# Kernel tuning notes

Hardware: AMD Instinct MI355X
Metric: run time of the kernel (lower is better)

Reference implementation:

```python
import jax, jax.numpy as jnp
import numpy as np

KH = KW = 3  # fixed: distortion() generates a 9-tap (3x3) offset grid


def make_offset(h, w, dilation=1.0, skydome=True):
    """Faithful numpy port of DistortionConvLayer.distortion -> [1,h,w,9,2] (last dim = [x_off, y_off])."""
    pi = np.pi
    unit_w = 2.0 * pi / w
    unit_h = pi / (2.0 * h) if skydome else pi / h
    rho = np.tan(unit_w) * dilation
    v = np.array([0.0, 1.0, 0.0])
    r_grid = np.array([[1, -1], [1, 0], [1, 1], [0, -1], [0, 0], [0, 1], [-1, -1], [-1, 0], [-1, 1]], dtype=np.float64)
    xc = int(w * 0.5)
    theta = (xc - 0.5 * w) * unit_w
    y = np.arange(h, dtype=np.float64)
    phi = (h - y) * unit_h if skydome else (h * 0.5 - y) * unit_h  # [h]
    p_u = np.stack([np.cos(phi) * np.cos(theta), np.sin(phi), np.cos(phi) * np.sin(theta)], axis=-1)  # [h,3]
    t_x = np.cross(np.broadcast_to(v, p_u.shape), p_u)  # [h,3]
    t_y = np.cross(p_u, t_x)                            # [h,3]
    # r_sphere: [h,9,3]
    r_sphere = rho * (r_grid[None, :, 0, None] * t_x[:, None, :] + r_grid[None, :, 1, None] * t_y[:, None, :])
    p_ur = p_u[:, None, :] + r_sphere  # [h,9,3]
    ux, uy, uz = p_ur[..., 0], p_ur[..., 1], p_ur[..., 2]
    base = np.arctan2(uz, ux)
    theta_r = np.where(ux > 0, base,
               np.where(ux < 0, np.where(uz >= 0, base + pi, base - pi),
                np.where(uz > 0, pi * 0.5, -pi * 0.5)))
    phi_r = np.arcsin(uy)
    x_r = (theta_r / pi + 1.0) * 0.5 * w
    y_r = (1.0 - 2.0 * phi_r / pi) * h if skydome else (0.5 - phi_r / pi) * h
    k = np.stack([x_r, y_r], axis=-1)          # [h,9,2], entries [x, y] (as in original)
    off = k - k[:, 4:5, :]                      # subtract center tap
    off = np.broadcast_to(off[:, None, :, :], (h, w, 9, 2))  # tile over width
    return off[None].astype(np.float32)         # [1,h,w,9,2]


def setup_inputs() -> dict:
    key = jax.random.key(0)
    k1, k2 = jax.random.split(key)
    B, H, W, C, F = 4, 128, 256, 64, 128
    inputs = jax.random.normal(k1, (B, H, W, C), dtype=jnp.float32)
    fan_in = KH * KW * C
    kernel = jax.random.normal(k2, (fan_in, F), dtype=jnp.float32) * (1.0 / np.sqrt(fan_in))
    bias = jnp.zeros((F,), dtype=jnp.float32)
    return {"inputs": inputs, "kernel": kernel, "bias": bias}


def reference(inputs, kernel, bias):
    B, H, W, C = inputs.shape
    F = kernel.shape[1]
    off = jnp.asarray(make_offset(H, W))  # [1,H,W,9,2], static constant
    # 'same' padding for 3x3, stride 1, dilation 1 -> pad 1 on each side
    xp = jnp.pad(inputs, ((0, 0), (1, 1), (1, 1), (0, 0)))
    in_h, in_w = H + 2, W + 2
    # base conv sampling coordinates (extract_patches order: tap k -> dy=k//3, dx=k%3)
    dy = jnp.repeat(jnp.arange(KH), KW).astype(jnp.float32)  # [9]
    dx = jnp.tile(jnp.arange(KW), KH).astype(jnp.float32)    # [9]
    base_y = jnp.arange(H, dtype=jnp.float32)[None, :, None, None] + dy[None, None, None, :]  # [1,H,1,9]
    base_x = jnp.arange(W, dtype=jnp.float32)[None, None, :, None] + dx[None, None, None, :]  # [1,1,W,9]
    # NOTE: faithful to original: channel 0 of offset (x_r diffs) is added to y, channel 1 to x
    y = base_y + off[..., 0]  # [1,H,W,9]
    x = base_x + off[..., 1]
    y = jnp.clip(y, 0.0, in_h - 1)
    x = jnp.where(x < 0, x + in_w, x)
    x = jnp.where(x > in_w - 1, x - in_w, x)
    y0 = jnp.floor(y).astype(jnp.int32)
    x0 = jnp.floor(x).astype(jnp.int32)
    y1, x1 = y0 + 1, x0 + 1
    y0 = jnp.clip(y0, 0, in_h - 1); y1 = jnp.clip(y1, 0, in_h - 1)
    x0 = jnp.clip(x0, 0, in_w - 1); x1 = jnp.clip(x1, 0, in_w - 1)
    bidx = jnp.arange(B)[:, None, None, None]  # [B,1,1,1], broadcasts against [1,H,W,9]
    gather = lambda yi, xi: xp[bidx, yi, xi]   # -> [B,H,W,9,C]
    p0 = gather(y0, x0); p1 = gather(y0, x1); p2 = gather(y1, x0); p3 = gather(y1, x1)
    y0f, y1f = y0.astype(jnp.float32), y1.astype(jnp.float32)
    x0f, x1f = x0.astype(jnp.float32), x1.astype(jnp.float32)
    w0 = ((y1f - y) * (x1f - x))[..., None]
    w1 = ((y1f - y) * (x - x0f))[..., None]
    w2 = ((y - y0f) * (x1f - x))[..., None]
    w3 = ((y - y0f) * (x - x0f))[..., None]
    pixels = w0 * p0 + w1 * p1 + w2 * p2 + w3 * p3  # [B,H,W,9,C]
    pixels = pixels.reshape(B, H * W, KH * KW * C)
    out = pixels @ kernel + bias                    # [B,HW,F]
    return jax.nn.relu(out.reshape(B, H, W, F))
```

## Files before the change

kernel.cpp:

```cpp
#include <hip/hip_runtime.h>
#include <math.h>

#define Bb 4
#define Hh 128
#define Ww 256
#define Cc 64
#define Ff 128
#define INH 130
#define INW 258

#define YSTRIDE 68
#define YSLOTS 37

typedef __attribute__((ext_vector_type(8))) __bf16 bf16x8;
typedef __attribute__((ext_vector_type(4))) float floatx4;

__device__ __forceinline__ unsigned short f2bf(float f) {
  unsigned int u = __float_as_uint(f);
  unsigned int r = u + 0x7fffu + ((u >> 16) & 1u);
  return (unsigned short)(r >> 16);
}

__device__ __forceinline__ unsigned int cvt_pk_bf16(float lo, float hi) {
  unsigned int r;
  asm("v_cvt_pk_bf16_f32 %0, %1, %2" : "=v"(r) : "v"(lo), "v"(hi));
  return r;
}

__global__ void prep_kernel(const float* __restrict__ kmat,
                            float* __restrict__ offtab,
                            unsigned short* __restrict__ kTB) {
  int gid = blockIdx.x * 256 + threadIdx.x;
  if (gid < 576 * 128) {
    int f = gid & 127;
    int k = gid >> 7;
    int tap = k >> 6;
    int r = k & 63;
    int kk = r >> 5;
    int quad = (r >> 3) & 3;
    int i = r & 7;
    int chunk = tap * 8 + kk * 4 + quad;
    kTB[((size_t)chunk * 128 + f) * 8 + i] = f2bf(kmat[gid]);
  }
  if (gid < Hh * 9) {
    int h = gid / 9;
    int j = gid - h * 9;
    const double pi = 3.14159265358979323846;
    double unit_w = 2.0 * pi / (double)Ww;
    double unit_h = pi / (2.0 * (double)Hh);
    double rho = tan(unit_w);
    double theta = ((double)(Ww / 2) - 0.5 * (double)Ww) * unit_w;
    double phi = ((double)Hh - (double)h) * unit_h;
    double cph = cos(phi), sph = sin(phi);
    double cth = cos(theta), sth = sin(theta);
    double pux = cph * cth, puy = sph, puz = cph * sth;
    double txx = puz, txy = 0.0, txz = -pux;
    double tyx = puy * txz - puz * txy;
    double tyy = puz * txx - pux * txz;
    double tyz = pux * txy - puy * txx;
    const int r0t[9] = {1, 1, 1, 0, 0, 0, -1, -1, -1};
    const int r1t[9] = {-1, 0, 1, -1, 0, 1, -1, 0, 1};
    auto proj = [&](int r0, int r1, double& xr, double& yr) {
      double ux = pux + rho * ((double)r0 * txx + (double)r1 * tyx);
      double uy = puy + rho * ((double)r0 * txy + (double)r1 * tyy);
      double uz = puz + rho * ((double)r0 * txz + (double)r1 * tyz);
      double base = atan2(uz, ux);
      double th;
      if (ux > 0.0)        th = base;
      else if (ux < 0.0)   th = (uz >= 0.0) ? base + pi : base - pi;
      else                 th = (uz > 0.0) ? pi * 0.5 : -pi * 0.5;
      double ph = asin(uy);
      xr = (th / pi + 1.0) * 0.5 * (double)Ww;
      yr = (1.0 - 2.0 * ph / pi) * (double)Hh;
    };
    double xc, yc, xj, yj;
    proj(0, 0, xc, yc);
    proj(r0t[j], r1t[j], xj, yj);
    offtab[gid * 2 + 0] = (float)(xj - xc);
    offtab[gid * 2 + 1] = (float)(yj - yc);
  }
}

__global__ __launch_bounds__(256, 4) void fused_kernel(
    const float* __restrict__ in, const float* __restrict__ bias,
    const unsigned short* __restrict__ kTB, const float* __restrict__ offtab,
    float* __restrict__ out) {
  __shared__ float ybH[4 * YSLOTS * YSTRIDE];

  int lidx = ((blockIdx.x & 7) << 7) | (blockIdx.x >> 3);
  int wt = lidx & 1;
  int h  = (lidx >> 1) & 127;
  int b  = lidx >> 8;
  int w0 = wt << 7;

  int tid  = threadIdx.x;
  int lane = tid & 63;
  int wave = tid >> 6;
  int m_base = wave << 5;
  int l15  = lane & 15;
  int quad = lane >> 4;

  float* yb = &ybH[wave * (YSLOTS * YSTRIDE)];
  if (lane < 17) *(float4*)&yb[36 * YSTRIDE + lane * 4] = (float4){0.f, 0.f, 0.f, 0.f};

  floatx4 acc[2][8];
#pragma unroll
  for (int i = 0; i < 2; i++)
#pragma unroll
    for (int j = 0; j < 8; j++) acc[i][j] = (floatx4){0.f, 0.f, 0.f, 0.f};

  const float* inb = in + (size_t)b * Hh * Ww * Cc;
  const bf16x8* kbase = (const bf16x8*)kTB;

  for (int tap = 0; tap < 9; tap++) {
    float off0 = offtab[(h * 9 + tap) * 2 + 0];
    float off1 = offtab[(h * 9 + tap) * 2 + 1];
    float dyk = (float)(tap / 3), dxk = (float)(tap % 3);

    float y = (float)h + dyk + off0;
    y = fminf(fmaxf(y, 0.f), (float)(INH - 1));
    int y0i = (int)floorf(y);
    int y1i = y0i + 1;
    y0i = min(max(y0i, 0), INH - 1);
    y1i = min(max(y1i, 0), INH - 1);
    float wy0 = (float)y1i - y;
    float wy1 = y - (float)y0i;
    if (!(y0i >= 1 && y0i <= Hh)) wy0 = 0.f;
    if (!(y1i >= 1 && y1i <= Hh)) wy1 = 0.f;
    const char* r0 = (const char*)(inb + (size_t)min(max(y0i - 1, 0), Hh - 1) * Ww * Cc);
    const char* r1 = (const char*)(inb + (size_t)min(max(y1i - 1, 0), Hh - 1) * Ww * Cc);

    float xrep = (float)w0 + dxk + off1;
    float flo  = floorf(xrep);
    int jb = (int)flo - 1;
    float fr = xrep - flo;
    float fxa = 1.f - fr, fxb = fr;

    int s0v[2], s1v[2];
#pragma unroll
    for (int mi = 0; mi < 2; mi++) {
      int wr = m_base + mi * 16 + l15;
      float x = (float)(w0 + wr) + dxk + off1;
      if (x < 0.f) x += (float)INW;
      if (x > (float)(INW - 1)) x -= (float)INW;
      int x0i = (int)floorf(x);
      int s = x0i - jb;
      if (s < 0) s += INW;
      int ls = s - m_base;
      bool ok = (unsigned)ls <= 34u;
      s0v[mi] = ok ? ls : 36;
      s1v[mi] = ok ? ls + 1 : 36;
    }

#pragma unroll
    for (int it = 0; it < 5; it++) {
      int t = lane + (it << 6);
      if (it < 4 || lane < 32) {
        int ls = t >> 3;
        int c8f = (t & 7) << 3;
        int col = jb + m_base + ls;
        if (col < 0) col += INW;
        if (col > INW - 1) col -= INW;
        bool cok = ((unsigned)(col - 1) < (unsigned)Ww);
        unsigned offc = (((unsigned)((col - 1) & (Ww - 1))) << 8) + ((unsigned)c8f << 2);
        float wa = cok ? wy0 : 0.f;
        float wb = cok ? wy1 : 0.f;
        float4 a0 = *(const float4*)(r0 + offc);
        float4 a1 = *(const float4*)(r0 + offc + 16);
        float4 b0 = *(const float4*)(r1 + offc);
        float4 b1 = *(const float4*)(r1 + offc + 16);
        float4 p0, p1;
        p0.x = wa * a0.x + wb * b0.x;
        p0.y = wa * a0.y + wb * b0.y;
        p0.z = wa * a0.z + wb * b0.z;
        p0.w = wa * a0.w + wb * b0.w;
        p1.x = wa * a1.x + wb * b1.x;
        p1.y = wa * a1.y + wb * b1.y;
        p1.z = wa * a1.z + wb * b1.z;
        p1.w = wa * a1.w + wb * b1.w;
        float* dst = yb + ls * YSTRIDE + c8f;
        *(float4*)dst = p0;
        *(float4*)(dst + 4) = p1;
      }
    }

#pragma unroll
    for (int kk = 0; kk < 2; kk++) {
      int ch0 = (tap * 8 + kk * 4 + quad) * 128;
      bf16x8 af[2];
#pragma unroll
      for (int mi = 0; mi < 2; mi++) {
        const float* pa = yb + s0v[mi] * YSTRIDE + kk * 32 + quad * 8;
        const float* pb = yb + s1v[mi] * YSTRIDE + kk * 32 + quad * 8;
        float4 ya = *(const float4*)pa;
        float4 yA = *(const float4*)(pa + 4);
        float4 yc = *(const float4*)pb;
        float4 yC = *(const float4*)(pb + 4);
        float p0 = fxa * ya.x + fxb * yc.x;
        float p1 = fxa * ya.y + fxb * yc.y;
        float p2 = fxa * ya.z + fxb * yc.z;
        float p3 = fxa * ya.w + fxb * yc.w;
        float p4 = fxa * yA.x + fxb * yC.x;
        float p5 = fxa * yA.y + fxb * yC.y;
        float p6 = fxa * yA.z + fxb * yC.z;
        float p7 = fxa * yA.w + fxb * yC.w;
        union { uint4 u; bf16x8 v; } afc;
        afc.u.x = cvt_pk_bf16(p0, p1);
        afc.u.y = cvt_pk_bf16(p2, p3);
        afc.u.z = cvt_pk_bf16(p4, p5);
        afc.u.w = cvt_pk_bf16(p6, p7);
        af[mi] = afc.v;
      }
#pragma unroll
      for (int ni = 0; ni < 8; ni++) {
        bf16x8 bf = kbase[ch0 + ni * 16 + l15];
        acc[0][ni] = __builtin_amdgcn_mfma_f32_16x16x32_bf16(af[0], bf, acc[0][ni], 0, 0, 0);
        acc[1][ni] = __builtin_amdgcn_mfma_f32_16x16x32_bf16(af[1], bf, acc[1][ni], 0, 0, 0);
      }
    }
  }

  size_t outbase = ((size_t)(b * Hh + h) * Ww + w0);
#pragma unroll
  for (int ni = 0; ni < 8; ni++) {
    int f = ni * 16 + l15;
    float bv = bias[f];
#pragma unroll
    for (int mi = 0; mi < 2; mi++) {
#pragma unroll
      for (int r = 0; r < 4; r++) {
        int m = m_base + mi * 16 + quad * 4 + r;
        out[(outbase + m) * Ff + f] = fmaxf(acc[mi][ni][r] + bv, 0.f);
      }
    }
  }
}

extern "C" void kernel_launch(void* const* d_in, const int* in_sizes, int n_in,
                              void* d_out, int out_size, void* d_ws, size_t ws_size,
                              hipStream_t stream) {
  const float* in   = (const float*)d_in[0];
  const float* kmat = (const float*)d_in[1];
  const float* bias = (const float*)d_in[2];
  float* out = (float*)d_out;

  float* offtab = (float*)d_ws;
  unsigned short* kTB = (unsigned short*)((char*)d_ws + Hh * 9 * 2 * sizeof(float));
  if (ws_size < (size_t)(Hh * 9 * 2 * sizeof(float) + 128 * 576 * sizeof(unsigned short)))
    return;

  prep_kernel<<<288, 256, 0, stream>>>(kmat, offtab, kTB);
  fused_kernel<<<Bb * Hh * (Ww / 128), 256, 0, stream>>>(in, bias, kTB, offtab, out);
}
```

Measured before the change: 136.6 us.

## Split taps across wave pairs, store bf16 staging window, reduce via LDS

Each block now covers 64 output columns instead of 128. Its four waves are arranged as two row groups times two tap groups: one tap group handles taps 0-4 and the other taps 5-8. The partial accumulators are summed through shared memory in four chunks before bias and ReLU are applied. The vertical-interpolation staging buffer is now stored as bf16 instead of fp32, which halves LDS use, and launch bounds rise to allow more resident blocks. B fragments are loaded ahead of the MFMAs. The trade-off is extra LDS reduction traffic, barriers, an uneven 5/4 tap split, and an additional bf16 rounding of the intermediate values.

```diff
diff --git a/kernel.cpp b/kernel.cpp
--- a/kernel.cpp
+++ b/kernel.cpp
@@ -9,8 +9,8 @@
 #define INH 130
 #define INW 258
 
-#define YSTRIDE 68
-#define YSLOTS 37
+#define WSLOT 72
+#define WPW 37
 
 typedef __attribute__((ext_vector_type(8))) __bf16 bf16x8;
 typedef __attribute__((ext_vector_type(4))) float floatx4;
@@ -81,27 +81,29 @@
   }
 }
 
-__global__ __launch_bounds__(256, 4) void fused_kernel(
+__global__ __launch_bounds__(256, 7) void fused_kernel(
     const float* __restrict__ in, const float* __restrict__ bias,
     const unsigned short* __restrict__ kTB, const float* __restrict__ offtab,
     float* __restrict__ out) {
-  __shared__ float ybH[4 * YSLOTS * YSTRIDE];
-
-  int lidx = ((blockIdx.x & 7) << 7) | (blockIdx.x >> 3);
-  int wt = lidx & 1;
-  int h  = (lidx >> 1) & 127;
-  int b  = lidx >> 8;
-  int w0 = wt << 7;
+  __shared__ unsigned short winH[4 * WPW * WSLOT];
+
+  int lidx = ((blockIdx.x & 7) << 8) | (blockIdx.x >> 3);
+  int wt = lidx & 3;
+  int h  = (lidx >> 2) & 127;
+  int b  = lidx >> 9;
+  int w0 = wt << 6;
 
   int tid  = threadIdx.x;
   int lane = tid & 63;
   int wave = tid >> 6;
-  int m_base = wave << 5;
+  int mr   = wave & 1;
+  int tg   = wave >> 1;
+  int m_base = mr << 5;
   int l15  = lane & 15;
   int quad = lane >> 4;
 
-  float* yb = &ybH[wave * (YSLOTS * YSTRIDE)];
-  if (lane < 17) *(float4*)&yb[36 * YSTRIDE + lane * 4] = (float4){0.f, 0.f, 0.f, 0.f};
+  unsigned short* win = &winH[wave * (WPW * WSLOT)];
+  if (lane < 9) *(uint4*)&win[36 * WSLOT + lane * 8] = (uint4){0u, 0u, 0u, 0u};
 
   floatx4 acc[2][8];
 #pragma unroll
@@ -112,7 +114,9 @@
   const float* inb = in + (size_t)b * Hh * Ww * Cc;
   const bf16x8* kbase = (const bf16x8*)kTB;
 
-  for (int tap = 0; tap < 9; tap++) {
+  int tapA = tg ? 5 : 0;
+  int tapB = tg ? 9 : 5;
+  for (int tap = tapA; tap < tapB; tap++) {
     float off0 = offtab[(h * 9 + tap) * 2 + 0];
     float off1 = offtab[(h * 9 + tap) * 2 + 1];
     float dyk = (float)(tap / 3), dxk = (float)(tap % 3);
@@ -169,69 +173,86 @@
         float4 a1 = *(const float4*)(r0 + offc + 16);
         float4 b0 = *(const float4*)(r1 + offc);
         float4 b1 = *(const float4*)(r1 + offc + 16);
-        float4 p0, p1;
-        p0.x = wa * a0.x + wb * b0.x;
-        p0.y = wa * a0.y + wb * b0.y;
-        p0.z = wa * a0.z + wb * b0.z;
-        p0.w = wa * a0.w + wb * b0.w;
-        p1.x = wa * a1.x + wb * b1.x;
-        p1.y = wa * a1.y + wb * b1.y;
-        p1.z = wa * a1.z + wb * b1.z;
-        p1.w = wa * a1.w + wb * b1.w;
-        float* dst = yb + ls * YSTRIDE + c8f;
-        *(float4*)dst = p0;
-        *(float4*)(dst + 4) = p1;
+        uint4 st;
+        st.x = cvt_pk_bf16(wa * a0.x + wb * b0.x, wa * a0.y + wb * b0.y);
+        st.y = cvt_pk_bf16(wa * a0.z + wb * b0.z, wa * a0.w + wb * b0.w);
+        st.z = cvt_pk_bf16(wa * a1.x + wb * b1.x, wa * a1.y + wb * b1.y);
+        st.w = cvt_pk_bf16(wa * a1.z + wb * b1.z, wa * a1.w + wb * b1.w);
+        *(uint4*)(&win[ls * WSLOT + ((t & 7) << 3)]) = st;
       }
     }
 
 #pragma unroll
     for (int kk = 0; kk < 2; kk++) {
       int ch0 = (tap * 8 + kk * 4 + quad) * 128;
+      bf16x8 bfrag[8];
+#pragma unroll
+      for (int ni = 0; ni < 8; ni++)
+        bfrag[ni] = kbase[ch0 + ni * 16 + l15];
       bf16x8 af[2];
 #pragma unroll
       for (int mi = 0; mi < 2; mi++) {
-        const float* pa = yb + s0v[mi] * YSTRIDE + kk * 32 + quad * 8;
-        const float* pb = yb + s1v[mi] * YSTRIDE + kk * 32 + quad * 8;
-        float4 ya = *(const float4*)pa;
-        float4 yA = *(const float4*)(pa + 4);
-        float4 yc = *(const float4*)pb;
-        float4 yC = *(const float4*)(pb + 4);
-        float p0 = fxa * ya.x + fxb * yc.x;
-        float p1 = fxa * ya.y + fxb * yc.y;
-        float p2 = fxa * ya.z + fxb * yc.z;
-        float p3 = fxa * ya.w + fxb * yc.w;
-        float p4 = fxa * yA.x + fxb * yC.x;
-        float p5 = fxa * yA.y + fxb * yC.y;
-        float p6 = fxa * yA.z + fxb * yC.z;
-        float p7 = fxa * yA.w + fxb * yC.w;
+        uint4 ua = *(const uint4*)&win[s0v[mi] * WSLOT + kk * 32 + quad * 8];
+        uint4 ub = *(const uint4*)&win[s1v[mi] * WSLOT + kk * 32 + quad * 8];
         union { uint4 u; bf16x8 v; } afc;
-        afc.u.x = cvt_pk_bf16(p0, p1);
-        afc.u.y = cvt_pk_bf16(p2, p3);
-        afc.u.z = cvt_pk_bf16(p4, p5);
-        afc.u.w = cvt_pk_bf16(p6, p7);
+        {
+          float a0 = __uint_as_float(ua.x << 16), a1 = __uint_as_float(ua.x & 0xffff0000u);
+          float c0 = __uint_as_float(ub.x << 16), c1 = __uint_as_float(ub.x & 0xffff0000u);
+          afc.u.x = cvt_pk_bf16(fxa * a0 + fxb * c0, fxa * a1 + fxb * c1);
+        }
+        {
+          float a0 = __uint_as_float(ua.y << 16), a1 = __uint_as_float(ua.y & 0xffff0000u);
+          float c0 = __uint_as_float(ub.y << 16), c1 = __uint_as_float(ub.y & 0xffff0000u);
+          afc.u.y = cvt_pk_bf16(fxa * a0 + fxb * c0, fxa * a1 + fxb * c1);
+        }
+        {
+          float a0 = __uint_as_float(ua.z << 16), a1 = __uint_as_float(ua.z & 0xffff0000u);
+          float c0 = __uint_as_float(ub.z << 16), c1 = __uint_as_float(ub.z & 0xffff0000u);
+          afc.u.z = cvt_pk_bf16(fxa * a0 + fxb * c0, fxa * a1 + fxb * c1);
+        }
+        {
+          float a0 = __uint_as_float(ua.w << 16), a1 = __uint_as_float(ua.w & 0xffff0000u);
+          float c0 = __uint_as_float(ub.w << 16), c1 = __uint_as_float(ub.w & 0xffff0000u);
+          afc.u.w = cvt_pk_bf16(fxa * a0 + fxb * c0, fxa * a1 + fxb * c1);
+        }
         af[mi] = afc.v;
       }
 #pragma unroll
       for (int ni = 0; ni < 8; ni++) {
-        bf16x8 bf = kbase[ch0 + ni * 16 + l15];
-        acc[0][ni] = __builtin_amdgcn_mfma_f32_16x16x32_bf16(af[0], bf, acc[0][ni], 0, 0, 0);
-        acc[1][ni] = __builtin_amdgcn_mfma_f32_16x16x32_bf16(af[1], bf, acc[1][ni], 0, 0, 0);
+        acc[0][ni] = __builtin_amdgcn_mfma_f32_16x16x32_bf16(af[0], bfrag[ni], acc[0][ni], 0, 0, 0);
+        acc[1][ni] = __builtin_amdgcn_mfma_f32_16x16x32_bf16(af[1], bfrag[ni], acc[1][ni], 0, 0, 0);
       }
     }
   }
 
+  float* redbuf = (float*)&winH[(2 + mr) * (WPW * WSLOT)];
   size_t outbase = ((size_t)(b * Hh + h) * Ww + w0);
 #pragma unroll
-  for (int ni = 0; ni < 8; ni++) {
-    int f = ni * 16 + l15;
-    float bv = bias[f];
-#pragma unroll
-    for (int mi = 0; mi < 2; mi++) {
-#pragma unroll
-      for (int r = 0; r < 4; r++) {
-        int m = m_base + mi * 16 + quad * 4 + r;
-        out[(outbase + m) * Ff + f] = fmaxf(acc[mi][ni][r] + bv, 0.f);
-      }
+  for (int c = 0; c < 4; c++) {
+    __syncthreads();
+    if (tg == 1) {
+#pragma unroll
+      for (int mi = 0; mi < 2; mi++)
+#pragma unroll
+        for (int j = 0; j < 2; j++)
+          *(floatx4*)&redbuf[(mi * 2 + j) * 256 + lane * 4] = acc[mi][2 * c + j];
+    }
+    __syncthreads();
+    if (tg == 0) {
+#pragma unroll
+      for (int mi = 0; mi < 2; mi++)
+#pragma unroll
+        for (int j = 0; j < 2; j++) {
+          floatx4 other = *(const floatx4*)&redbuf[(mi * 2 + j) * 256 + lane * 4];
+          int ni = 2 * c + j;
+          int f = ni * 16 + l15;
+          float bv = bias[f];
+#pragma unroll
+          for (int r = 0; r < 4; r++) {
+            int m = m_base + mi * 16 + quad * 4 + r;
+            out[(outbase + m) * Ff + f] = fmaxf(acc[mi][ni][r] + other[r] + bv, 0.f);
+          }
+        }
     }
   }
 }
@@ -250,5 +271,5 @@
     return;
 
   prep_kernel<<<288, 256, 0, stream>>>(kmat, offtab, kTB);
-  fused_kernel<<<Bb * Hh * (Ww / 128), 256, 0, stream>>>(in, bias, kTB, offtab, out);
-}
+  fused_kernel<<<Bb * Hh * (Ww / 64), 256, 0, stream>>>(in, bias, kTB, offtab, out);
+}
```

Result: slower. 444.1 us (+225.0%).
